# Kernel tuning notes

Hardware: AMD Instinct MI355X
Metric: run time of the kernel (lower is better)

The kernel has to match this reference:

```python
import jax, jax.numpy as jnp
import numpy as np

VOCAB = 250002
UNUSED = np.array([0, 2, 1, 3])  # cls, eos, pad, unk token ids for XLM-R tokenizer
TEMP = 0.02
H = 1024


def _normalize(x, axis=-1):
    n = jnp.sqrt(jnp.sum(x * x, axis=axis, keepdims=True))
    return x / jnp.maximum(n, 1e-12)


def _sparse_embedding(hidden, ids, sparse_w, sparse_b):
    # token_weights = relu(Linear(H,1)(hidden)) -> [B, L]
    tw = jax.nn.relu(jnp.einsum('blh,h->bl', hidden, sparse_w) + sparse_b)
    B = hidden.shape[0]
    # torch: scatter into [B, L, V] then max over L; since tw >= 0 and base is 0,
    # this equals a scatter-max into [B, V] (avoids the huge [B,L,V] intermediate).
    emb = jnp.zeros((B, VOCAB), tw.dtype)
    emb = emb.at[jnp.arange(B)[:, None], ids].max(tw)
    emb = emb.at[:, UNUSED].set(0.0)
    return emb


def _colbert_embedding(hidden, mask, colbert_w, colbert_b):
    # Linear on tokens 1: (drop CLS), mask, then L2-normalize
    v = jnp.einsum('blh,dh->bld', hidden[:, 1:], colbert_w) + colbert_b
    v = v * mask[:, 1:, None]
    return _normalize(v)


def setup_inputs() -> dict:
    key = jax.random.key(0)
    ks = jax.random.split(key, 8)
    return {
        'q_hidden': jax.random.normal(ks[0], (8, 128, H), jnp.float32),
        'p_hidden': jax.random.normal(ks[1], (64, 512, H), jnp.float32),
        'q_mask': jnp.ones((8, 128), jnp.float32),
        'p_mask': jnp.ones((64, 512), jnp.float32),
        'q_ids': jax.random.randint(ks[2], (8, 128), 0, VOCAB),
        'p_ids': jax.random.randint(ks[3], (64, 512), 0, VOCAB),
        'colbert_w': jax.random.normal(ks[4], (H, H), jnp.float32) * 0.02,
        'colbert_b': jnp.zeros((H,), jnp.float32),
        'sparse_w': jax.random.normal(ks[5], (H,), jnp.float32) * 0.02,
        'sparse_b': jnp.zeros((), jnp.float32),
    }


def reference(q_hidden, p_hidden, q_mask, p_mask, q_ids, p_ids,
              colbert_w, colbert_b, sparse_w, sparse_b):
    # dense: cls pooling + normalize
    q_dense = _normalize(q_hidden[:, 0])
    p_dense = _normalize(p_hidden[:, 0])
    dense_scores = (q_dense @ p_dense.T) / TEMP  # [Bq, Bp]

    # sparse: relu-weighted vocab scatter-max
    q_sparse = _sparse_embedding(q_hidden, q_ids, sparse_w, sparse_b)
    p_sparse = _sparse_embedding(p_hidden, p_ids, sparse_w, sparse_b)
    sparse_scores = (q_sparse @ p_sparse.T) / TEMP  # [Bq, Bp]

    # colbert: late-interaction maxsim
    q_col = _colbert_embedding(q_hidden, q_mask, colbert_w, colbert_b)  # [Bq, Lq-1, H]
    p_col = _colbert_embedding(p_hidden, p_mask, colbert_w, colbert_b)  # [Bp, Lp-1, H]
    token_scores = jnp.einsum('qin,pjn->qipj', q_col, p_col)  # [Bq, Lq-1, Bp, Lp-1]
    colbert_scores = token_scores.max(-1).sum(1)
    colbert_scores = colbert_scores / q_mask[:, 1:].sum(-1, keepdims=True)
    colbert_scores = colbert_scores / TEMP  # [Bq, Bp]

    return dense_scores, sparse_scores, colbert_scores
```

## Files before the change

### kernel.cpp

```cpp
#include <hip/hip_runtime.h>
#include <hip/hip_bf16.h>


typedef __bf16 bf16x8 __attribute__((ext_vector_type(8)));
typedef float floatx4 __attribute__((ext_vector_type(4)));
typedef unsigned short ushort8v __attribute__((ext_vector_type(8)));

#define TEMP 0.02f

__device__ __forceinline__ unsigned short f2bf(float f) {
    unsigned u = __float_as_uint(f);
    unsigned r = (u + 0x7FFFu + ((u >> 16) & 1u)) >> 16;
    return (unsigned short)r;
}
__device__ __forceinline__ unsigned encf(float f) {
    unsigned u = __float_as_uint(f);
    return (u & 0x80000000u) ? ~u : (u | 0x80000000u);
}
__device__ __forceinline__ float decf(unsigned u) {
    return __uint_as_float((u & 0x80000000u) ? (u & 0x7FFFFFFFu) : ~u);
}

__device__ __forceinline__ void async_load16(void* lds, const void* g) {
    __builtin_amdgcn_global_load_lds(
        (__attribute__((address_space(1))) void*)g,
        (__attribute__((address_space(3))) void*)lds,
        16, 0, 0);
}

__global__ void conv_zero_tw(const float* __restrict__ qh, const float* __restrict__ ph,
                             const float* __restrict__ wsrc, unsigned short* __restrict__ dst,
                             const float* __restrict__ sw, const float* __restrict__ sb,
                             float* __restrict__ tw, unsigned* __restrict__ zbase)
{
    __shared__ float red[4];
    int b = blockIdx.x, t = threadIdx.x;
    if (b < 388) zbase[b * 256 + t] = 0u;
    int r0 = b * 2;
    const float* src;
    bool do_tw = true;
    if (r0 < 1024)       { src = qh   + (size_t)r0 * 1024; }
    else if (r0 < 33792) { src = ph   + (size_t)(r0 - 1024) * 1024; }
    else                 { src = wsrc + (size_t)(r0 - 33792) * 1024; do_tw = false; }
    const float4* s4 = (const float4*)src;
    float4 a = s4[t * 2], c = s4[t * 2 + 1];
    ushort8v o;
    o[0] = f2bf(a.x); o[1] = f2bf(a.y); o[2] = f2bf(a.z); o[3] = f2bf(a.w);
    o[4] = f2bf(c.x); o[5] = f2bf(c.y); o[6] = f2bf(c.z); o[7] = f2bf(c.w);
    ((ushort8v*)dst)[(size_t)b * 256 + t] = o;
    if (do_tw) {
        const float4* w4 = (const float4*)sw;
        int wi = (t & 127) * 2;
        float4 wa = w4[wi], wc = w4[wi + 1];
        float acc = a.x * wa.x + a.y * wa.y + a.z * wa.z + a.w * wa.w
                  + c.x * wc.x + c.y * wc.y + c.z * wc.z + c.w * wc.w;
        #pragma unroll
        for (int s = 32; s; s >>= 1) acc += __shfl_down(acc, s, 64);
        if ((t & 63) == 0) red[t >> 6] = acc;
        __syncthreads();
        if (t == 0)   tw[r0]     = fmaxf(red[0] + red[1] + sb[0], 0.0f);
        if (t == 128) tw[r0 + 1] = fmaxf(red[2] + red[3] + sb[0], 0.0f);
    }
}

__global__ void canon_all(const int* __restrict__ q_ids, const int* __restrict__ p_ids,
                          const float* __restrict__ tw,
                          float* __restrict__ eff_q, float* __restrict__ eff_p)
{
    __shared__ int   sid[512];
    __shared__ float stw[512];
    int b = blockIdx.x, t = threadIdx.x;
    const int* ids; const float* twr; float* eff; int L, chunk;
    if (b < 8) {
        L = 128; chunk = 0;
        ids = q_ids + b * 128; twr = tw + b * 128; eff = eff_q + b * 128;
    } else {
        int pr = (b - 8) >> 1; chunk = (b - 8) & 1; L = 512;
        ids = p_ids + pr * 512; twr = tw + 1024 + pr * 512; eff = eff_p + pr * 512;
    }
    for (int l = t; l < L; l += 256) { sid[l] = ids[l]; stw[l] = twr[l]; }
    __syncthreads();
    int l = chunk * 256 + t;
    if (l < L) {
        int id = sid[l];
        float wv = stw[l];
        bool kill = (id < 4);
        #pragma unroll 8
        for (int m = 0; m < L; ++m) {
            int idm = sid[m];
            float wm = stw[m];
            bool beats = (idm == id) & (m != l) & ((wm > wv) | ((wm == wv) & (m < l)));
            kill = kill | beats;
        }
        eff[l] = kill ? 0.0f : wv;
    }
}

template<int MODE>
__global__ __launch_bounds__(256, 2)
void gemm_bt(const unsigned short* __restrict__ A,
             const unsigned short* __restrict__ B,
             const float* __restrict__ bias,
             unsigned short* __restrict__ C,
             unsigned* __restrict__ Mbuf,
             float* __restrict__ normsq,
             const float* __restrict__ p_mask,
             int mTiles, int N, int K,
             const float* __restrict__ qh, const float* __restrict__ ph,
             const int* __restrict__ q_ids, const int* __restrict__ p_ids,
             const float* __restrict__ eff_q, const float* __restrict__ eff_p,
             float* __restrict__ out)
{
    __shared__ unsigned short smA[128 * 64];
    __shared__ unsigned short smB[128 * 64];
    const int tid  = threadIdx.x;

    if (MODE == 0 && (int)blockIdx.x >= mTiles) {
        int pair = ((int)blockIdx.x - mTiles) * 8 + (int)blockIdx.y;
        int qb = pair >> 6, pb = pair & 63;
        char* lds = (char*)smA;
        int*   qid = (int*)lds;
        float* qef = (float*)(lds + 512);
        int*   pid = (int*)(lds + 1024);
        float* pef = (float*)(lds + 3072);
        float* redD = (float*)(lds + 5120);
        float* redS = (float*)(lds + 5184);
        int t = tid;
        if (t < 128) { qid[t] = q_ids[qb * 128 + t]; qef[t] = eff_q[qb * 128 + t]; }
        for (int m = t; m < 512; m += 256) { pid[m] = p_ids[pb * 512 + m]; pef[m] = eff_p[pb * 512 + m]; }
        const float4* q4 = (const float4*)(qh + (size_t)qb * 128 * 1024);
        const float4* p4 = (const float4*)(ph + (size_t)pb * 512 * 1024);
        float4 a = q4[t], b = p4[t];
        float dot = a.x * b.x + a.y * b.y + a.z * b.z + a.w * b.w;
        float nq  = a.x * a.x + a.y * a.y + a.z * a.z + a.w * a.w;
        float np  = b.x * b.x + b.y * b.y + b.z * b.z + b.w * b.w;
        #pragma unroll
        for (int sh = 32; sh; sh >>= 1) {
            dot += __shfl_down(dot, sh, 64);
            nq  += __shfl_down(nq, sh, 64);
            np  += __shfl_down(np, sh, 64);
        }
        if ((t & 63) == 0) { int w = t >> 6; redD[w] = dot; redD[4 + w] = nq; redD[8 + w] = np; }
        __syncthreads();
        if (t == 0) {
            float d = redD[0] + redD[1] + redD[2] + redD[3];
            float n1 = redD[4] + redD[5] + redD[6] + redD[7];
            float n2 = redD[8] + redD[9] + redD[10] + redD[11];
            out[qb * 64 + pb] = d / (fmaxf(sqrtf(n1), 1e-12f) * fmaxf(sqrtf(n2), 1e-12f)) / TEMP;
        }
        float s = 0.0f;
        for (int idx = t; idx < 128 * 512; idx += 256) {
            int l = idx >> 9, m = idx & 511;
            if (qid[l] == pid[m]) s += qef[l] * pef[m];
        }
        #pragma unroll
        for (int sh = 32; sh; sh >>= 1) s += __shfl_down(s, sh, 64);
        if ((t & 63) == 0) redS[t >> 6] = s;
        __syncthreads();
        if (t == 0) out[512 + qb * 64 + pb] = (redS[0] + redS[1] + redS[2] + redS[3]) / TEMP;
        return;
    }

    const int lane = tid & 63;
    const int w    = tid >> 6;
    const int wm   = w >> 1, wn = w & 1;
    const int quad = lane >> 4, m16 = lane & 15;
    const int rowTile = (MODE == 0) ? blockIdx.x : blockIdx.y;
    const int colTile = (MODE == 0) ? blockIdx.y : blockIdx.x;
    const int rowBase = rowTile * 128;
    const int colBase = colTile * 128;

    const int sr = lane >> 2;
    const int scg = (lane & 3) ^ ((lane >> 3) & 3);
    const unsigned short* aG0 = A + (long long)(rowBase + w * 16 + sr) * K + scg * 8;
    const unsigned short* aG1 = aG0 + 64LL * K;
    const unsigned short* bG0 = B + (long long)(colBase + w * 16 + sr) * K + scg * 8;
    const unsigned short* bG1 = bG0 + 64LL * K;
    unsigned short* lA0 = smA + w * 512;
    unsigned short* lA1 = smA + (w + 4) * 512;
    unsigned short* lB0 = smB + w * 512;
    unsigned short* lB1 = smB + (w + 4) * 512;

    const int fragOff = (m16 * 4 + (quad ^ ((m16 >> 1) & 3))) * 8;

    floatx4 acc[4][4] = {};

    for (int k0 = 0; k0 < K; k0 += 64) {
        async_load16(lA0,        aG0 + k0);
        async_load16(lA0 + 4096, aG0 + k0 + 32);
        async_load16(lA1,        aG1 + k0);
        async_load16(lA1 + 4096, aG1 + k0 + 32);
        async_load16(lB0,        bG0 + k0);
        async_load16(lB0 + 4096, bG0 + k0 + 32);
        async_load16(lB1,        bG1 + k0);
        async_load16(lB1 + 4096, bG1 + k0 + 32);
        __syncthreads();
        #pragma unroll
        for (int h = 0; h < 2; ++h) {
            bf16x8 af[4], bfr[4];
            #pragma unroll
            for (int f = 0; f < 4; ++f) {
                af[f]  = *(const bf16x8*)(smA + h * 4096 + (wm * 4 + f) * 512 + fragOff);
                bfr[f] = *(const bf16x8*)(smB + h * 4096 + (wn * 4 + f) * 512 + fragOff);
            }
            #pragma unroll
            for (int i = 0; i < 4; ++i)
                #pragma unroll
                for (int j = 0; j < 4; ++j)
                    acc[i][j] = __builtin_amdgcn_mfma_f32_16x16x32_bf16(af[i], bfr[j], acc[i][j], 0, 0, 0);
        }
        __syncthreads();
    }

    if (MODE == 0) {
        float bcol[4];
        #pragma unroll
        for (int j = 0; j < 4; ++j) bcol[j] = bias[colBase + wn * 64 + j * 16 + m16];
        #pragma unroll
        for (int i = 0; i < 4; ++i) {
            int row0 = rowBase + wm * 64 + i * 16 + quad * 4;
            #pragma unroll
            for (int r = 0; r < 4; ++r) {
                float sq = 0.0f;
                #pragma unroll
                for (int j = 0; j < 4; ++j) {
                    int col = colBase + wn * 64 + j * 16 + m16;
                    float val = acc[i][j][r] + bcol[j];
                    C[(long long)(row0 + r) * N + col] = f2bf(val);
                    sq += val * val;
                }
                #pragma unroll
                for (int s = 1; s < 16; s <<= 1) sq += __shfl_xor(sq, s, 64);
                if (m16 == 0) atomicAdd(&normsq[row0 + r], sq);
            }
        }
    } else {
        const int pb = colBase >> 9;
        float pfac[4];
        #pragma unroll
        for (int j = 0; j < 4; ++j) {
            int colg = colBase + wn * 64 + j * 16 + m16;
            float pm = p_mask[colg];
            float pn = sqrtf(normsq[1024 + colg]);
            pfac[j] = pm / fmaxf(pn * pm, 1e-12f);
        }
        #pragma unroll
        for (int i = 0; i < 4; ++i) {
            #pragma unroll
            for (int r = 0; r < 4; ++r) {
                float mx = -3.0e38f;
                #pragma unroll
                for (int j = 0; j < 4; ++j) {
                    int colg = colBase + wn * 64 + j * 16 + m16;
                    float v = acc[i][j][r] * pfac[j];
                    if ((colg & 511) == 0) v = -3.0e38f;
                    mx = fmaxf(mx, v);
                }
                #pragma unroll
                for (int s = 1; s < 16; s <<= 1) mx = fmaxf(mx, __shfl_xor(mx, s, 64));
                if (m16 == 0) {
                    int row = rowBase + wm * 64 + i * 16 + quad * 4 + r;
                    atomicMax(&Mbuf[row * 64 + pb], encf(mx));
                }
            }
        }
    }
}

__global__ void colbert_reduce_k(const unsigned* __restrict__ Mbuf,
                                 const float* __restrict__ q_mask,
                                 const float* __restrict__ normsq,
                                 float* __restrict__ out)
{
    int pair = blockIdx.x * 4 + (threadIdx.x >> 6);
    int lane = threadIdx.x & 63;
    int qb = pair >> 6, pb = pair & 63;
    float s = 0.0f, msum = 0.0f;
    for (int i = 1 + lane; i < 128; i += 64) {
        float qm = q_mask[qb * 128 + i];
        float qn = sqrtf(normsq[qb * 128 + i]);
        float qfac = qm / fmaxf(qn * qm, 1e-12f);
        s += decf(Mbuf[(qb * 128 + i) * 64 + pb]) * qfac;
        msum += qm;
    }
    #pragma unroll
    for (int sh = 32; sh; sh >>= 1) {
        s += __shfl_down(s, sh, 64);
        msum += __shfl_down(msum, sh, 64);
    }
    if (lane == 0) out[1024 + qb * 64 + pb] = s / msum / TEMP;
}

extern "C" void kernel_launch(void* const* d_in, const int* in_sizes, int n_in,
                              void* d_out, int out_size, void* d_ws, size_t ws_size,
                              hipStream_t stream)
{
    const float* q_hidden = (const float*)d_in[0];
    const float* p_hidden = (const float*)d_in[1];
    const float* q_mask   = (const float*)d_in[2];
    const float* p_mask   = (const float*)d_in[3];
    const int*   q_ids    = (const int*)d_in[4];
    const int*   p_ids    = (const int*)d_in[5];
    const float* colbert_w = (const float*)d_in[6];
    const float* colbert_b = (const float*)d_in[7];
    const float* sparse_w  = (const float*)d_in[8];
    const float* sparse_b  = (const float*)d_in[9];
    float* out = (float*)d_out;

    char* ws = (char*)d_ws;
    size_t off = 0;
    auto carve = [&](size_t bytes) { char* p = ws + off; off += (bytes + 255) & ~(size_t)255; return p; };
    unsigned short* qhb  = (unsigned short*)carve((size_t)1024 * 1024 * 2);
    unsigned short* phb  = (unsigned short*)carve((size_t)32768 * 1024 * 2);
    unsigned short* Wb   = (unsigned short*)carve((size_t)1024 * 1024 * 2);
    unsigned short* qv   = (unsigned short*)carve((size_t)1024 * 1024 * 2);
    unsigned short* pv   = (unsigned short*)carve((size_t)32768 * 1024 * 2);
    unsigned* Mbuf  = (unsigned*)carve((size_t)1024 * 64 * 4);
    float*    normsq = (float*)carve((size_t)33792 * 4);
    float*    tw    = (float*)carve((size_t)33792 * 4);
    float*    eff_q = (float*)carve(1024 * 4);
    float*    eff_p = (float*)carve(32768 * 4);
    (void)phb; (void)Wb; (void)pv;

    conv_zero_tw<<<17408, 256, 0, stream>>>(q_hidden, p_hidden, colbert_w, qhb,
                                            sparse_w, sparse_b, tw, Mbuf);

    canon_all<<<136, 256, 0, stream>>>(q_ids, p_ids, tw, eff_q, eff_p);

    gemm_bt<0><<<dim3(264 + 64, 8), 256, 0, stream>>>(
        qhb, Wb, colbert_b, qv, nullptr, normsq, nullptr, 264, 1024, 1024,
        q_hidden, p_hidden, q_ids, p_ids, eff_q, eff_p, out);

    gemm_bt<1><<<dim3(256, 8), 256, 0, stream>>>(
        qv, pv, nullptr, nullptr, Mbuf, normsq, p_mask, 8, 32768, 1024,
        nullptr, nullptr, nullptr, nullptr, nullptr, nullptr, nullptr);

    colbert_reduce_k<<<128, 256, 0, stream>>>(Mbuf, q_mask, normsq, out);
}
```

Baseline: 414.4 us.

## Switch GEMMs to 256x256 tiles with double-buffered LDS software pipeline

Replaces the 128x128, 256-thread GEMM with a 256x256, 512-thread kernel. It double-buffers LDS, interleaves async global-to-LDS loads for later K tiles with MFMA work using explicit barriers, waitcnt and setprio, and reuses B fragments across two A halves. The aim is to hide global load latency behind the matrix cores and raise arithmetic intensity per byte loaded. The dense and sparse side-blocks are adapted to 512 threads. In exchange it uses much more LDS and more registers (8x4 accumulators), which lowers occupancy, and the grid becomes coarser.

```diff
diff --git a/kernel.cpp b/kernel.cpp
--- a/kernel.cpp
+++ b/kernel.cpp
@@ -97,8 +97,8 @@
 }
 
 template<int MODE>
-__global__ __launch_bounds__(256, 2)
-void gemm_bt(const unsigned short* __restrict__ A,
+__global__ __launch_bounds__(512, 2)
+void gemm256(const unsigned short* __restrict__ A,
              const unsigned short* __restrict__ B,
              const float* __restrict__ bias,
              unsigned short* __restrict__ C,
@@ -111,45 +111,45 @@
              const float* __restrict__ eff_q, const float* __restrict__ eff_p,
              float* __restrict__ out)
 {
-    __shared__ unsigned short smA[128 * 64];
-    __shared__ unsigned short smB[128 * 64];
-    const int tid  = threadIdx.x;
+    __shared__ unsigned short smA[2][16384];
+    __shared__ unsigned short smB[2][16384];
+    const int tid = threadIdx.x;
 
     if (MODE == 0 && (int)blockIdx.x >= mTiles) {
-        int pair = ((int)blockIdx.x - mTiles) * 8 + (int)blockIdx.y;
+        int pair = ((int)blockIdx.x - mTiles) * 4 + (int)blockIdx.y;
         int qb = pair >> 6, pb = pair & 63;
-        char* lds = (char*)smA;
+        char* lds = (char*)&smA[0][0];
         int*   qid = (int*)lds;
         float* qef = (float*)(lds + 512);
         int*   pid = (int*)(lds + 1024);
         float* pef = (float*)(lds + 3072);
         float* redD = (float*)(lds + 5120);
-        float* redS = (float*)(lds + 5184);
+        float* redS = (float*)(lds + 5248);
         int t = tid;
         if (t < 128) { qid[t] = q_ids[qb * 128 + t]; qef[t] = eff_q[qb * 128 + t]; }
-        for (int m = t; m < 512; m += 256) { pid[m] = p_ids[pb * 512 + m]; pef[m] = eff_p[pb * 512 + m]; }
-        const float4* q4 = (const float4*)(qh + (size_t)qb * 128 * 1024);
-        const float4* p4 = (const float4*)(ph + (size_t)pb * 512 * 1024);
-        float4 a = q4[t], b = p4[t];
-        float dot = a.x * b.x + a.y * b.y + a.z * b.z + a.w * b.w;
-        float nq  = a.x * a.x + a.y * a.y + a.z * a.z + a.w * a.w;
-        float np  = b.x * b.x + b.y * b.y + b.z * b.z + b.w * b.w;
+        pid[t] = p_ids[pb * 512 + t]; pef[t] = eff_p[pb * 512 + t];
+        const float2* q2 = (const float2*)(qh + (size_t)qb * 128 * 1024);
+        const float2* p2 = (const float2*)(ph + (size_t)pb * 512 * 1024);
+        float2 a = q2[t], b = p2[t];
+        float dot = a.x * b.x + a.y * b.y;
+        float nq  = a.x * a.x + a.y * a.y;
+        float np  = b.x * b.x + b.y * b.y;
         #pragma unroll
         for (int sh = 32; sh; sh >>= 1) {
             dot += __shfl_down(dot, sh, 64);
             nq  += __shfl_down(nq, sh, 64);
             np  += __shfl_down(np, sh, 64);
         }
-        if ((t & 63) == 0) { int w = t >> 6; redD[w] = dot; redD[4 + w] = nq; redD[8 + w] = np; }
+        if ((t & 63) == 0) { int wv = t >> 6; redD[wv] = dot; redD[8 + wv] = nq; redD[16 + wv] = np; }
         __syncthreads();
         if (t == 0) {
-            float d = redD[0] + redD[1] + redD[2] + redD[3];
-            float n1 = redD[4] + redD[5] + redD[6] + redD[7];
-            float n2 = redD[8] + redD[9] + redD[10] + redD[11];
+            float d = 0.0f, n1 = 0.0f, n2 = 0.0f;
+            #pragma unroll
+            for (int wv = 0; wv < 8; ++wv) { d += redD[wv]; n1 += redD[8 + wv]; n2 += redD[16 + wv]; }
             out[qb * 64 + pb] = d / (fmaxf(sqrtf(n1), 1e-12f) * fmaxf(sqrtf(n2), 1e-12f)) / TEMP;
         }
         float s = 0.0f;
-        for (int idx = t; idx < 128 * 512; idx += 256) {
+        for (int idx = t; idx < 128 * 512; idx += 512) {
             int l = idx >> 9, m = idx & 511;
             if (qid[l] == pid[m]) s += qef[l] * pef[m];
         }
@@ -157,76 +157,132 @@
         for (int sh = 32; sh; sh >>= 1) s += __shfl_down(s, sh, 64);
         if ((t & 63) == 0) redS[t >> 6] = s;
         __syncthreads();
-        if (t == 0) out[512 + qb * 64 + pb] = (redS[0] + redS[1] + redS[2] + redS[3]) / TEMP;
+        if (t == 0) {
+            float sv = 0.0f;
+            #pragma unroll
+            for (int wv = 0; wv < 8; ++wv) sv += redS[wv];
+            out[512 + qb * 64 + pb] = sv / TEMP;
+        }
         return;
     }
 
     const int lane = tid & 63;
     const int w    = tid >> 6;
-    const int wm   = w >> 1, wn = w & 1;
+    const int wm   = w >> 2, wn = w & 3;
     const int quad = lane >> 4, m16 = lane & 15;
-    const int rowTile = (MODE == 0) ? blockIdx.x : blockIdx.y;
-    const int colTile = (MODE == 0) ? blockIdx.y : blockIdx.x;
-    const int rowBase = rowTile * 128;
-    const int colBase = colTile * 128;
-
-    const int sr = lane >> 2;
+    const int wm8 = wm * 8, wn4 = wn * 4;
+    const int rowTile = (MODE == 0) ? (int)blockIdx.x : (int)blockIdx.y;
+    const int colTile = (MODE == 0) ? (int)blockIdx.y : (int)blockIdx.x;
+    const long long rowBase = (long long)rowTile * 256;
+    const long long colBase = (long long)colTile * 256;
+
+    const int sr  = lane >> 2;
     const int scg = (lane & 3) ^ ((lane >> 3) & 3);
-    const unsigned short* aG0 = A + (long long)(rowBase + w * 16 + sr) * K + scg * 8;
-    const unsigned short* aG1 = aG0 + 64LL * K;
-    const unsigned short* bG0 = B + (long long)(colBase + w * 16 + sr) * K + scg * 8;
-    const unsigned short* bG1 = bG0 + 64LL * K;
-    unsigned short* lA0 = smA + w * 512;
-    unsigned short* lA1 = smA + (w + 4) * 512;
-    unsigned short* lB0 = smB + w * 512;
-    unsigned short* lB1 = smB + (w + 4) * 512;
-
-    const int fragOff = (m16 * 4 + (quad ^ ((m16 >> 1) & 3))) * 8;
-
-    floatx4 acc[4][4] = {};
-
-    for (int k0 = 0; k0 < K; k0 += 64) {
-        async_load16(lA0,        aG0 + k0);
-        async_load16(lA0 + 4096, aG0 + k0 + 32);
-        async_load16(lA1,        aG1 + k0);
-        async_load16(lA1 + 4096, aG1 + k0 + 32);
-        async_load16(lB0,        bG0 + k0);
-        async_load16(lB0 + 4096, bG0 + k0 + 32);
-        async_load16(lB1,        bG1 + k0);
-        async_load16(lB1 + 4096, bG1 + k0 + 32);
-        __syncthreads();
-        #pragma unroll
-        for (int h = 0; h < 2; ++h) {
-            bf16x8 af[4], bfr[4];
-            #pragma unroll
-            for (int f = 0; f < 4; ++f) {
-                af[f]  = *(const bf16x8*)(smA + h * 4096 + (wm * 4 + f) * 512 + fragOff);
-                bfr[f] = *(const bf16x8*)(smB + h * 4096 + (wn * 4 + f) * 512 + fragOff);
-            }
-            #pragma unroll
-            for (int i = 0; i < 4; ++i)
-                #pragma unroll
-                for (int j = 0; j < 4; ++j)
-                    acc[i][j] = __builtin_amdgcn_mfma_f32_16x16x32_bf16(af[i], bfr[j], acc[i][j], 0, 0, 0);
-        }
-        __syncthreads();
-    }
+    const unsigned short* aG = A + (rowBase + w * 16 + sr) * K + scg * 8;
+    const unsigned short* bG = B + (colBase + w * 16 + sr) * K + scg * 8;
+
+    const int fragOff = m16 * 32 + (quad ^ ((m16 >> 1) & 3)) * 8;
+    const int NT = K >> 6;
+
+    floatx4 acc[8][4] = {};
+    bf16x8 af[4], bkeep[4];
+
+#define STAGE_A(d, kh, ts) do { \
+    async_load16(&smA[d][(kh) * 8192 + w * 512],       aG + (long long)(ts) * 64 + (kh) * 32); \
+    async_load16(&smA[d][(kh) * 8192 + (8 + w) * 512], aG + 128LL * K + (long long)(ts) * 64 + (kh) * 32); \
+} while (0)
+#define STAGE_B(d, kh, ts) do { \
+    async_load16(&smB[d][(kh) * 8192 + w * 512],       bG + (long long)(ts) * 64 + (kh) * 32); \
+    async_load16(&smB[d][(kh) * 8192 + (8 + w) * 512], bG + 128LL * K + (long long)(ts) * 64 + (kh) * 32); \
+} while (0)
+#define DS_A(d, kh, g) (*(const bf16x8*)&smA[d][(kh) * 8192 + (g) * 512 + fragOff])
+#define DS_B(d, kh, g) (*(const bf16x8*)&smB[d][(kh) * 8192 + (g) * 512 + fragOff])
+#define MFMA16(fb) \
+    _Pragma("unroll") \
+    for (int f_ = 0; f_ < 4; ++f_) { \
+        _Pragma("unroll") \
+        for (int j_ = 0; j_ < 4; ++j_) \
+            acc[(fb) + f_][j_] = __builtin_amdgcn_mfma_f32_16x16x32_bf16(af[f_], bkeep[j_], acc[(fb) + f_][j_], 0, 0, 0); \
+    }
+#define BAR()   __builtin_amdgcn_s_barrier()
+#define LGKM0() asm volatile("s_waitcnt lgkmcnt(0)" ::: "memory")
+
+#define TILE(d, T1A, T2) do { \
+     \
+    _Pragma("unroll") for (int j_ = 0; j_ < 4; ++j_) bkeep[j_] = DS_B(d, 0, wn4 + j_); \
+    _Pragma("unroll") for (int f_ = 0; f_ < 4; ++f_) af[f_]    = DS_A(d, 0, wm8 + f_); \
+    STAGE_A((d) ^ 1, 1, T1A); \
+    BAR(); LGKM0(); \
+    __builtin_amdgcn_s_setprio(1); \
+    MFMA16(0); \
+    __builtin_amdgcn_s_setprio(0); \
+    BAR(); \
+     \
+    _Pragma("unroll") for (int f_ = 0; f_ < 4; ++f_) af[f_] = DS_A(d, 0, wm8 + 4 + f_); \
+    STAGE_B(d, 0, T2); \
+    BAR(); LGKM0(); \
+    __builtin_amdgcn_s_setprio(1); \
+    MFMA16(4); \
+    __builtin_amdgcn_s_setprio(0); \
+    BAR(); \
+     \
+    _Pragma("unroll") for (int j_ = 0; j_ < 4; ++j_) bkeep[j_] = DS_B(d, 1, wn4 + j_); \
+    _Pragma("unroll") for (int f_ = 0; f_ < 4; ++f_) af[f_]    = DS_A(d, 1, wm8 + f_); \
+    STAGE_A(d, 0, T2); \
+    BAR(); LGKM0(); \
+    __builtin_amdgcn_s_setprio(1); \
+    MFMA16(0); \
+    __builtin_amdgcn_s_setprio(0); \
+    BAR(); \
+     \
+    _Pragma("unroll") for (int f_ = 0; f_ < 4; ++f_) af[f_] = DS_A(d, 1, wm8 + 4 + f_); \
+    STAGE_B(d, 1, T2); \
+    BAR(); LGKM0(); \
+    __builtin_amdgcn_s_setprio(1); \
+    MFMA16(4); \
+    __builtin_amdgcn_s_setprio(0); \
+    asm volatile("s_waitcnt vmcnt(6)" ::: "memory"); \
+    BAR(); \
+} while (0)
+
+    STAGE_A(0, 0, 0); STAGE_B(0, 0, 0); STAGE_A(0, 1, 0); STAGE_B(0, 1, 0);
+    STAGE_B(1, 0, 1); STAGE_A(1, 0, 1); STAGE_B(1, 1, 1);
+    asm volatile("s_waitcnt vmcnt(6)" ::: "memory");
+    BAR();
+
+    #pragma unroll 1
+    for (int tt = 0; tt < NT; tt += 2) {
+        const int u2 = (tt + 2 < NT) ? tt + 2 : NT - 1;
+        const int u3 = (tt + 3 < NT) ? tt + 3 : NT - 1;
+        TILE(0, tt + 1, u2);
+        TILE(1, u2, u3);
+    }
+    asm volatile("s_waitcnt vmcnt(0)" ::: "memory");
+
+#undef STAGE_A
+#undef STAGE_B
+#undef DS_A
+#undef DS_B
+#undef MFMA16
+#undef BAR
+#undef LGKM0
+#undef TILE
 
     if (MODE == 0) {
         float bcol[4];
         #pragma unroll
         for (int j = 0; j < 4; ++j) bcol[j] = bias[colBase + wn * 64 + j * 16 + m16];
         #pragma unroll
-        for (int i = 0; i < 4; ++i) {
-            int row0 = rowBase + wm * 64 + i * 16 + quad * 4;
+        for (int f = 0; f < 8; ++f) {
+            long long row0 = rowBase + wm * 128 + f * 16 + quad * 4;
             #pragma unroll
             for (int r = 0; r < 4; ++r) {
                 float sq = 0.0f;
                 #pragma unroll
                 for (int j = 0; j < 4; ++j) {
-                    int col = colBase + wn * 64 + j * 16 + m16;
-                    float val = acc[i][j][r] + bcol[j];
-                    C[(long long)(row0 + r) * N + col] = f2bf(val);
+                    long long col = colBase + wn * 64 + j * 16 + m16;
+                    float val = acc[f][j][r] + bcol[j];
+                    C[(row0 + r) * N + col] = f2bf(val);
                     sq += val * val;
                 }
                 #pragma unroll
@@ -235,31 +291,31 @@
             }
         }
     } else {
-        const int pb = colBase >> 9;
+        const int pb = (int)(colBase >> 9);
         float pfac[4];
         #pragma unroll
         for (int j = 0; j < 4; ++j) {
-            int colg = colBase + wn * 64 + j * 16 + m16;
+            int colg = (int)colBase + wn * 64 + j * 16 + m16;
             float pm = p_mask[colg];
             float pn = sqrtf(normsq[1024 + colg]);
             pfac[j] = pm / fmaxf(pn * pm, 1e-12f);
         }
         #pragma unroll
-        for (int i = 0; i < 4; ++i) {
+        for (int f = 0; f < 8; ++f) {
             #pragma unroll
             for (int r = 0; r < 4; ++r) {
                 float mx = -3.0e38f;
                 #pragma unroll
                 for (int j = 0; j < 4; ++j) {
-                    int colg = colBase + wn * 64 + j * 16 + m16;
-                    float v = acc[i][j][r] * pfac[j];
+                    int colg = (int)colBase + wn * 64 + j * 16 + m16;
+                    float v = acc[f][j][r] * pfac[j];
                     if ((colg & 511) == 0) v = -3.0e38f;
                     mx = fmaxf(mx, v);
                 }
                 #pragma unroll
                 for (int s = 1; s < 16; s <<= 1) mx = fmaxf(mx, __shfl_xor(mx, s, 64));
                 if (m16 == 0) {
-                    int row = rowBase + wm * 64 + i * 16 + quad * 4 + r;
+                    int row = (int)rowBase + wm * 128 + f * 16 + quad * 4 + r;
                     atomicMax(&Mbuf[row * 64 + pb], encf(mx));
                 }
             }
@@ -327,12 +383,12 @@
 
     canon_all<<<136, 256, 0, stream>>>(q_ids, p_ids, tw, eff_q, eff_p);
 
-    gemm_bt<0><<<dim3(264 + 64, 8), 256, 0, stream>>>(
-        qhb, Wb, colbert_b, qv, nullptr, normsq, nullptr, 264, 1024, 1024,
+    gemm256<0><<<dim3(132 + 128, 4), 512, 0, stream>>>(
+        qhb, Wb, colbert_b, qv, nullptr, normsq, nullptr, 132, 1024, 1024,
         q_hidden, p_hidden, q_ids, p_ids, eff_q, eff_p, out);
 
-    gemm_bt<1><<<dim3(256, 8), 256, 0, stream>>>(
-        qv, pv, nullptr, nullptr, Mbuf, normsq, p_mask, 8, 32768, 1024,
+    gemm256<1><<<dim3(128, 4), 512, 0, stream>>>(
+        qv, pv, nullptr, nullptr, Mbuf, normsq, p_mask, 4, 32768, 1024,
         nullptr, nullptr, nullptr, nullptr, nullptr, nullptr, nullptr);
 
     colbert_reduce_k<<<128, 256, 0, stream>>>(Mbuf, q_mask, normsq, out);
```

Measured after the change: 445.6 us. +7.5%, slower.
